# Performance work log

Measured on AMD Instinct MI355X. Metric: run time of the kernel, lower is better.

The kernel has to match this reference:

```python
import jax, jax.numpy as jnp
import numpy as np

# Dims: tokens [B,H,W,C]; 3x3 local window (NB=9 neighbors); relative-pos embed dim RP.
B, H, W, C = 4, 96, 96, 128
K, NB, RP = 3, 9, 8
HID = 128              # edge_hidden_dim = max(hidden_dim//2=128, feature_dim=128)
EDGE_IN = 3 * C + RP   # [center, neighbor, center-neighbor, rel_pos] -> 392
CLIP = 3.0
GATE_EPS = 1e-6
LN_EPS = 1e-5


def _ln(x, w, b):
    m = jnp.mean(x, axis=-1, keepdims=True)
    v = jnp.mean((x - m) ** 2, axis=-1, keepdims=True)
    return (x - m) * jax.lax.rsqrt(v + LN_EPS) * w + b


def _mlp(x, w1, b1, w2, b2):
    # Linear -> GELU (exact/erf, torch default) -> Linear; dropout is identity in eval mode.
    return jax.nn.gelu(x @ w1 + b1, approximate=False) @ w2 + b2


def _eml(drive, resistance, gamma_raw, lam, bias, warmup_eta):
    # EMLUnit energy gate (source not provided; Ohm's-law style drive/resistance,
    # positive resistance via softplus, clipped, warmup-scaled, learned bias).
    gamma = jax.nn.softplus(gamma_raw)
    conduct = drive / (jax.nn.softplus(resistance) + gamma + GATE_EPS)
    return warmup_eta * jnp.clip(lam * conduct, -CLIP, CLIP) + bias


def setup_inputs() -> dict:
    key = jax.random.key(0)
    ks = jax.random.split(key, 8)

    def w(k, shape, std=0.01):
        return jax.random.normal(k, shape, jnp.float32) * std

    return {
        "tokens": jax.random.normal(ks[0], (B, H, W, C), jnp.float32),
        "ln1_w": jnp.ones((C,), jnp.float32), "ln1_b": jnp.zeros((C,), jnp.float32),
        "ln2_w": jnp.ones((C,), jnp.float32), "ln2_b": jnp.zeros((C,), jnp.float32),
        "rel_pos": w(ks[1], (NB, RP), 0.02),
        "d_w1": w(ks[2], (EDGE_IN, HID)), "d_b1": jnp.zeros((HID,), jnp.float32),
        "d_w2": w(ks[3], (HID, 1)), "d_b2": jnp.zeros((1,), jnp.float32),
        "r_w1": w(ks[4], (EDGE_IN, HID)), "r_b1": jnp.zeros((HID,), jnp.float32),
        "r_w2": w(ks[5], (HID, 1)), "r_b2": jnp.zeros((1,), jnp.float32),
        "v_w": w(ks[6], (C, C)), "v_b": jnp.zeros((C,), jnp.float32),
        "o_w": w(ks[7], (C, C)), "o_b": jnp.zeros((C,), jnp.float32),
        "eml_gamma": jnp.full((1,), 0.1, jnp.float32),
        "eml_lam": jnp.ones((1,), jnp.float32),
        "eml_bias": jnp.full((1,), -0.3, jnp.float32),
    }


def reference(tokens, ln1_w, ln1_b, ln2_w, ln2_b, rel_pos,
              d_w1, d_b1, d_w2, d_b2, r_w1, r_b1, r_w2, r_b2,
              v_w, v_b, o_w, o_b, eml_gamma, eml_lam, eml_bias):
    b, h, w_, c = tokens.shape
    hw = h * w_
    norm = _ln(tokens, ln1_w, ln1_b)
    # nn.Unfold(kernel=3, padding=1): zero-pad then gather 3x3 windows (row-major ky,kx order).
    pad = jnp.pad(norm, ((0, 0), (1, 1), (1, 1), (0, 0)))
    neigh = jnp.stack([pad[:, dy:dy + h, dx:dx + w_, :]
                       for dy in range(K) for dx in range(K)], axis=3)  # [B,H,W,9,C]
    neigh = neigh.reshape(b, hw, NB, c)
    center = jnp.broadcast_to(norm.reshape(b, hw, 1, c), (b, hw, NB, c))
    relp = jnp.broadcast_to(rel_pos[None, None], (b, hw, NB, RP))
    edge = jnp.concatenate([center, neigh, center - neigh, relp], axis=-1)  # [B,HW,9,392]
    drive = _mlp(edge, d_w1, d_b1, d_w2, d_b2)[..., 0]        # [B,HW,9]
    resistance = _mlp(edge, r_w1, r_b1, r_w2, r_b2)[..., 0]   # [B,HW,9]
    energy = _eml(drive, resistance, eml_gamma, eml_lam, eml_bias, 1.0)
    gate = jax.nn.sigmoid(energy)[..., None]                  # [B,HW,9,1]
    values = neigh @ v_w + v_b                                # [B,HW,9,C]
    gate_mass = jnp.clip(jnp.sum(gate, axis=2), GATE_EPS, None)  # [B,HW,1]
    message = jnp.sum(gate * values, axis=2) / gate_mass      # [B,HW,C]
    update = (message @ o_w + o_b).reshape(b, h, w_, c)
    return _ln(tokens + update, ln2_w, ln2_b)
```

## Files before the change

kernel.cpp:

```cpp
#include <hip/hip_runtime.h>
#include <stdint.h>

#define NPIX 36864

using bf16x8 = __attribute__((ext_vector_type(8))) short;
using f32x4  = __attribute__((ext_vector_type(4))) float;

__device__ __forceinline__ float bf2f(uint16_t u){
  return __uint_as_float(((uint32_t)u) << 16);
}
__device__ __forceinline__ float bl(uint32_t u){ return __uint_as_float(u << 16); }
__device__ __forceinline__ float bh(uint32_t u){ return __uint_as_float(u & 0xFFFF0000u); }
__device__ __forceinline__ uint16_t f2bf(float f){
  uint32_t u = __float_as_uint(f);
  u += 0x7fffu + ((u >> 16) & 1u);
  return (uint16_t)(u >> 16);
}
__device__ __forceinline__ float ldw(const void* p, int i, bool f32){
  return f32 ? ((const float*)p)[i] : bf2f(((const uint16_t*)p)[i]);
}
__device__ __forceinline__ bool probe_f32(const void* ones_vec){
  return ((const uint32_t*)ones_vec)[0] == 0x3F800000u;
}
__device__ __forceinline__ float geluf(float x){
  float u = x * x;
  float t = x * fmaf(u, 0.0713548162f, 1.5957691216f);
  t = fminf(fmaxf(t, -30.f), 30.f);
  float e = __expf(t);
  return x * e * __builtin_amdgcn_rcpf(e + 1.0f);
}
__device__ __forceinline__ float softplusf(float x){
  return fmaxf(x, 0.f) + __logf(1.f + __expf(-fabsf(x)));
}
__device__ __forceinline__ void acc2(float& acc, uint32_t c, uint32_t n,
                                     float r0, float r1, float w0, float w1){
  acc = fmaf(geluf(bl(c) + bl(n) + r0), w0, acc);
  acc = fmaf(geluf(bh(c) + bh(n) + r1), w1, acc);
}

__global__ void prep_kernel(const void* __restrict__ dw1, const void* __restrict__ rw1,
                            const void* __restrict__ vw,  const void* __restrict__ relp,
                            const void* __restrict__ db1, const void* __restrict__ rb1,
                            const void* __restrict__ ow,  const void* __restrict__ probe,
                            const void* __restrict__ dw2, const void* __restrict__ rw2,
                            const void* __restrict__ vb,  const void* __restrict__ db2,
                            const void* __restrict__ rb2, const void* __restrict__ eg,
                            const void* __restrict__ el,  const void* __restrict__ eb,
                            uint16_t* __restrict__ wcatT, float* __restrict__ Rd,
                            float* __restrict__ Rr, uint16_t* __restrict__ owT,
                            float* __restrict__ w2df, float* __restrict__ w2rf,
                            float* __restrict__ vbf, float* __restrict__ sc){
  const bool F = probe_f32(probe);
  const int j = blockIdx.x;
  const int c = threadIdx.x;
  if (j < 640){
    float val;
    if (j < 128)      val = ldw(dw1, c*128 + j, F)             + ldw(dw1, (256+c)*128 + j, F);
    else if (j < 256) val = ldw(dw1, (128+c)*128 + (j-128), F) - ldw(dw1, (256+c)*128 + (j-128), F);
    else if (j < 384) val = ldw(rw1, c*128 + (j-256), F)       + ldw(rw1, (256+c)*128 + (j-256), F);
    else if (j < 512) val = ldw(rw1, (128+c)*128 + (j-384), F) - ldw(rw1, (256+c)*128 + (j-384), F);
    else              val = ldw(vw, c*128 + (j-512), F);
    wcatT[j*128 + c] = f2bf(val);
  } else if (j < 649){
    const int k = j - 640;
    float sd = ldw(db1, c, F);
    float sr = ldw(rb1, c, F);
    #pragma unroll
    for (int r = 0; r < 8; ++r){
      float rp = ldw(relp, k*8 + r, F);
      sd += rp * ldw(dw1, (384+r)*128 + c, F);
      sr += rp * ldw(rw1, (384+r)*128 + c, F);
    }
    Rd[k*128 + c] = sd;
    Rr[k*128 + c] = sr;
  } else if (j < 777){
    const int n = j - 649;
    owT[n*128 + c] = f2bf(ldw(ow, c*128 + n, F));
  } else {
    w2df[c] = ldw(dw2, c, F);
    w2rf[c] = ldw(rw2, c, F);
    vbf[c]  = ldw(vb, c, F);
    if (c == 0){
      sc[0] = ldw(db2, 0, F);
      sc[1] = ldw(rb2, 0, F);
      sc[2] = softplusf(ldw(eg, 0, F));
      sc[3] = ldw(el, 0, F);
      sc[4] = ldw(eb, 0, F);
    }
  }
}

__global__ __launch_bounds__(256) void ln1_kernel(const void* __restrict__ tokens,
                                                  const void* __restrict__ w,
                                                  const void* __restrict__ b,
                                                  uint16_t* __restrict__ norm){
  const bool F = probe_f32(w);
  const int wv = threadIdx.x >> 6, lane = threadIdx.x & 63;
  const int p = blockIdx.x * 4 + wv;
  float f0, f1;
  if (F){
    const float2 t = ((const float2*)tokens)[(size_t)p*64 + lane];
    f0 = t.x; f1 = t.y;
  } else {
    const uint32_t pk = ((const uint32_t*)tokens)[(size_t)p*64 + lane];
    f0 = bl(pk); f1 = bh(pk);
  }
  float s = f0 + f1;
  #pragma unroll
  for (int m = 1; m < 64; m <<= 1) s += __shfl_xor(s, m, 64);
  const float mean = s * (1.f/128.f);
  const float d0 = f0 - mean, d1 = f1 - mean;
  float q = d0*d0 + d1*d1;
  #pragma unroll
  for (int m = 1; m < 64; m <<= 1) q += __shfl_xor(q, m, 64);
  const float rs = rsqrtf(q * (1.f/128.f) + 1e-5f);
  const float n0 = d0*rs*ldw(w, 2*lane, F)   + ldw(b, 2*lane, F);
  const float n1 = d1*rs*ldw(w, 2*lane+1, F) + ldw(b, 2*lane+1, F);
  ((uint32_t*)(norm + (size_t)p*128))[lane] = (uint32_t)f2bf(n0) | ((uint32_t)f2bf(n1) << 16);
}

__global__ __launch_bounds__(256) void gemm1_kernel(const uint16_t* __restrict__ A,
                                                    const uint16_t* __restrict__ BT,
                                                    uint16_t* __restrict__ PT,
                                                    uint16_t* __restrict__ V){
  __shared__ __align__(16) uint16_t As[128*128];
  __shared__ __align__(16) uint16_t Bs[128*128];
  const int row0 = blockIdx.x * 128;
  const int s    = blockIdx.y;
  const int col0 = s * 128;
  const int t = threadIdx.x;
  #pragma unroll
  for (int i = 0; i < 8; ++i){
    int cid = t + i*256;
    int r = cid >> 4, c8 = cid & 15;
    int scz = c8 ^ (r & 15);
    *(uint4*)&As[r*128 + scz*8] = *(const uint4*)&A[(size_t)(row0+r)*128 + c8*8];
    *(uint4*)&Bs[r*128 + scz*8] = *(const uint4*)&BT[(size_t)(col0+r)*128 + c8*8];
  }
  __syncthreads();
  const int wv = t >> 6, lane = t & 63;
  const int wr = (wv >> 1) * 64, wc = (wv & 1) * 64;
  const int lr = lane & 15, quad = lane >> 4;
  f32x4 acc[4][4] = {};
  #pragma unroll
  for (int kk = 0; kk < 4; ++kk){
    const int chunk = kk*4 + quad;
    bf16x8 a[4], b[4];
    #pragma unroll
    for (int mi = 0; mi < 4; ++mi){
      int r = wr + mi*16 + lr;
      a[mi] = *(const bf16x8*)&As[r*128 + (chunk ^ (r & 15))*8];
    }
    #pragma unroll
    for (int ni = 0; ni < 4; ++ni){
      int r = wc + ni*16 + lr;
      b[ni] = *(const bf16x8*)&Bs[r*128 + (chunk ^ (r & 15))*8];
    }
    #pragma unroll
    for (int mi = 0; mi < 4; ++mi)
      #pragma unroll
      for (int ni = 0; ni < 4; ++ni)
        acc[mi][ni] = __builtin_amdgcn_mfma_f32_16x16x32_bf16(a[mi], b[ni], acc[mi][ni], 0, 0, 0);
  }
  #pragma unroll
  for (int mi = 0; mi < 4; ++mi){
    #pragma unroll
    for (int ni = 0; ni < 4; ++ni){
      const int ch   = wc + ni*16 + lr;
      const int rowb = row0 + wr + mi*16 + quad*4;
      #pragma unroll
      for (int r = 0; r < 4; ++r){
        const uint16_t vbf16 = f2bf(acc[mi][ni][r]);
        if (s < 4)
          PT[((size_t)(s*16 + (ch >> 3))*NPIX + (rowb + r))*8 + (ch & 7)] = vbf16;
        else
          V[(size_t)(rowb + r)*128 + ch] = vbf16;
      }
    }
  }
}

__global__ __launch_bounds__(192) void edge_kernel(const uint16_t* __restrict__ PTraw,
    const float* __restrict__ Rd, const float* __restrict__ Rr,
    const float* __restrict__ w2df, const float* __restrict__ w2rf,
    const float* __restrict__ sc, float* __restrict__ gates){
  const int wv = __builtin_amdgcn_readfirstlane(threadIdx.x >> 6);
  const int lane = threadIdx.x & 63;
  const int k = blockIdx.y * 3 + wv;
  const int p = blockIdx.x * 64 + lane;
  const int dy = k/3 - 1, dx = k%3 - 1;
  const int x = p % 96, y = (p / 96) % 96;
  const bool inb = ((unsigned)(x + dx) < 96u) && ((unsigned)(y + dy) < 96u);
  const uint32_t m = inb ? 0xFFFFFFFFu : 0u;
  const int q = inb ? (p + dy*96 + dx) : p;
  const uint4* PT4 = (const uint4*)PTraw;
  const float4* rd4 = (const float4*)(Rd + k*128);
  const float4* rr4 = (const float4*)(Rr + k*128);
  const float4* wd4 = (const float4*)w2df;
  const float4* wr4 = (const float4*)w2rf;
  float accd = 0.f, accr = 0.f;
  #pragma unroll 4
  for (int i = 0; i < 16; ++i){
    uint4 cd = PT4[(size_t)( 0 + i)*NPIX + p];
    uint4 nd = PT4[(size_t)(16 + i)*NPIX + q];
    uint4 cr = PT4[(size_t)(32 + i)*NPIX + p];
    uint4 nr = PT4[(size_t)(48 + i)*NPIX + q];
    nd.x &= m; nd.y &= m; nd.z &= m; nd.w &= m;
    nr.x &= m; nr.y &= m; nr.z &= m; nr.w &= m;
    const float4 rdA = rd4[2*i], rdB = rd4[2*i+1];
    const float4 rrA = rr4[2*i], rrB = rr4[2*i+1];
    const float4 wdA = wd4[2*i], wdB = wd4[2*i+1];
    const float4 wrA = wr4[2*i], wrB = wr4[2*i+1];
    acc2(accd, cd.x, nd.x, rdA.x, rdA.y, wdA.x, wdA.y);
    acc2(accd, cd.y, nd.y, rdA.z, rdA.w, wdA.z, wdA.w);
    acc2(accd, cd.z, nd.z, rdB.x, rdB.y, wdB.x, wdB.y);
    acc2(accd, cd.w, nd.w, rdB.z, rdB.w, wdB.z, wdB.w);
    acc2(accr, cr.x, nr.x, rrA.x, rrA.y, wrA.x, wrA.y);
    acc2(accr, cr.y, nr.y, rrA.z, rrA.w, wrA.z, wrA.w);
    acc2(accr, cr.z, nr.z, rrB.x, rrB.y, wrB.x, wrB.y);
    acc2(accr, cr.w, nr.w, rrB.z, rrB.w, wrB.z, wrB.w);
  }
  const float drive  = accd + sc[0];
  const float resist = accr + sc[1];
  const float cond = __fdividef(drive, softplusf(resist) + sc[2] + 1e-6f);
  const float en = fminf(fmaxf(sc[3] * cond, -3.0f), 3.0f) + sc[4];
  const float g = __fdividef(1.0f, 1.0f + __expf(-en));
  gates[(size_t)k*NPIX + p] = g;
}

__global__ __launch_bounds__(256) void msg_kernel(const uint16_t* __restrict__ V,
    const float* __restrict__ gates, const float* __restrict__ vbf,
    uint16_t* __restrict__ msg){
  const int wv = __builtin_amdgcn_readfirstlane(threadIdx.x >> 6);
  const int lane = threadIdx.x & 63;
  const int p = blockIdx.x * 4 + wv;
  const int x = p % 96, y = (p / 96) % 96;
  float g[9], gsum = 0.f;
  #pragma unroll
  for (int k = 0; k < 9; ++k){ g[k] = gates[(size_t)k*NPIX + p]; gsum += g[k]; }
  float a0 = 0.f, a1 = 0.f;
  #pragma unroll
  for (int k = 0; k < 9; ++k){
    const int dy = k/3 - 1, dx = k%3 - 1;
    if (((unsigned)(y + dy) < 96u) && ((unsigned)(x + dx) < 96u)){
      const uint32_t u = ((const uint32_t*)(V + (size_t)(p + dy*96 + dx)*128))[lane];
      a0 = fmaf(g[k], bl(u), a0);
      a1 = fmaf(g[k], bh(u), a1);
    }
  }
  const float2 vb2 = ((const float2*)vbf)[lane];
  const float inv = __fdividef(1.0f, fmaxf(gsum, 1e-6f));
  a0 = (a0 + gsum * vb2.x) * inv;
  a1 = (a1 + gsum * vb2.y) * inv;
  ((uint32_t*)(msg + (size_t)p*128))[lane] = (uint32_t)f2bf(a0) | ((uint32_t)f2bf(a1) << 16);
}

__global__ __launch_bounds__(256) void out_kernel(const uint16_t* __restrict__ Amsg,
    const uint16_t* __restrict__ owT, const void* __restrict__ tokens,
    const void* __restrict__ ob,  const void* __restrict__ ln2w,
    const void* __restrict__ ln2b, void* __restrict__ out){
  const bool F = probe_f32(ln2w);
  __shared__ __align__(16) char smem[65536];
  uint16_t* As = (uint16_t*)smem;
  uint16_t* Bs = (uint16_t*)(smem + 32768);
  float*    U  = (float*)smem;
  const int row0 = blockIdx.x * 128;
  const int t = threadIdx.x;
  #pragma unroll
  for (int i = 0; i < 8; ++i){
    int cid = t + i*256;
    int r = cid >> 4, c8 = cid & 15;
    int scz = c8 ^ (r & 15);
    *(uint4*)&As[r*128 + scz*8] = *(const uint4*)&Amsg[(size_t)(row0+r)*128 + c8*8];
    *(uint4*)&Bs[r*128 + scz*8] = *(const uint4*)&owT[(size_t)r*128 + c8*8];
  }
  __syncthreads();
  const int wv = t >> 6, lane = t & 63;
  const int wr = (wv >> 1) * 64, wc = (wv & 1) * 64;
  const int lr = lane & 15, quad = lane >> 4;
  f32x4 acc[4][4] = {};
  #pragma unroll
  for (int kk = 0; kk < 4; ++kk){
    const int chunk = kk*4 + quad;
    bf16x8 a[4], b[4];
    #pragma unroll
    for (int mi = 0; mi < 4; ++mi){
      int r = wr + mi*16 + lr;
      a[mi] = *(const bf16x8*)&As[r*128 + (chunk ^ (r & 15))*8];
    }
    #pragma unroll
    for (int ni = 0; ni < 4; ++ni){
      int r = wc + ni*16 + lr;
      b[ni] = *(const bf16x8*)&Bs[r*128 + (chunk ^ (r & 15))*8];
    }
    #pragma unroll
    for (int mi = 0; mi < 4; ++mi)
      #pragma unroll
      for (int ni = 0; ni < 4; ++ni)
        acc[mi][ni] = __builtin_amdgcn_mfma_f32_16x16x32_bf16(a[mi], b[ni], acc[mi][ni], 0, 0, 0);
  }
  __syncthreads();
  #pragma unroll
  for (int mi = 0; mi < 4; ++mi)
    #pragma unroll
    for (int ni = 0; ni < 4; ++ni)
      #pragma unroll
      for (int r = 0; r < 4; ++r)
        U[(wr + mi*16 + quad*4 + r)*128 + (wc + ni*16 + lr)] = acc[mi][ni][r];
  __syncthreads();
  const float lw0 = ldw(ln2w, 2*lane, F), lw1 = ldw(ln2w, 2*lane+1, F);
  const float lb0 = ldw(ln2b, 2*lane, F), lb1 = ldw(ln2b, 2*lane+1, F);
  const float ob0 = ldw(ob, 2*lane, F),   ob1 = ldw(ob, 2*lane+1, F);
  for (int rr = 0; rr < 32; ++rr){
    const int row = wv*32 + rr;
    const int p = row0 + row;
    const float2 uv = ((const float2*)U)[row*64 + lane];
    float t0, t1;
    if (F){
      const float2 tk = ((const float2*)tokens)[(size_t)p*64 + lane];
      t0 = tk.x; t1 = tk.y;
    } else {
      const uint32_t tk = ((const uint32_t*)tokens)[(size_t)p*64 + lane];
      t0 = bl(tk); t1 = bh(tk);
    }
    const float a0 = uv.x + ob0 + t0;
    const float a1 = uv.y + ob1 + t1;
    float s = a0 + a1;
    #pragma unroll
    for (int m = 1; m < 64; m <<= 1) s += __shfl_xor(s, m, 64);
    const float mean = s * (1.f/128.f);
    const float d0 = a0 - mean, d1 = a1 - mean;
    float q = d0*d0 + d1*d1;
    #pragma unroll
    for (int m = 1; m < 64; m <<= 1) q += __shfl_xor(q, m, 64);
    const float rs = rsqrtf(q * (1.f/128.f) + 1e-5f);
    const float o0 = d0*rs*lw0 + lb0;
    const float o1 = d1*rs*lw1 + lb1;
    if (F){
      ((float2*)out)[(size_t)p*64 + lane] = make_float2(o0, o1);
    } else {
      ((uint32_t*)out)[(size_t)p*64 + lane] = (uint32_t)f2bf(o0) | ((uint32_t)f2bf(o1) << 16);
    }
  }
}

extern "C" void kernel_launch(void* const* d_in, const int* in_sizes, int n_in,
                              void* d_out, int out_size, void* d_ws, size_t ws_size,
                              hipStream_t stream) {
  const void* tokens = d_in[0];
  const void* ln1w   = d_in[1];
  const void* ln1b   = d_in[2];
  const void* ln2w   = d_in[3];
  const void* ln2b   = d_in[4];
  const void* relp   = d_in[5];
  const void* dw1    = d_in[6];
  const void* db1    = d_in[7];
  const void* dw2    = d_in[8];
  const void* db2    = d_in[9];
  const void* rw1    = d_in[10];
  const void* rb1    = d_in[11];
  const void* rw2    = d_in[12];
  const void* rb2    = d_in[13];
  const void* vw     = d_in[14];
  const void* vb     = d_in[15];
  const void* ow     = d_in[16];
  const void* ob     = d_in[17];
  const void* eg     = d_in[18];
  const void* el     = d_in[19];
  const void* eb     = d_in[20];

  char* ws = (char*)d_ws;
  uint16_t* normb = (uint16_t*)(ws + 0);
  uint16_t* PT    = (uint16_t*)(ws + 9437184);
  uint16_t* V     = (uint16_t*)(ws + 47185920);
  float*    gates = (float*)   (ws + 56623104);
  uint16_t* wcatT = (uint16_t*)(ws + 57950208);
  float*    Rd    = (float*)   (ws + 58114048);
  float*    Rr    = (float*)   (ws + 58118656);
  uint16_t* owT   = (uint16_t*)(ws + 58123264);
  float*    w2df  = (float*)   (ws + 58156032);
  float*    w2rf  = (float*)   (ws + 58156544);
  float*    vbf   = (float*)   (ws + 58157056);
  float*    sc    = (float*)   (ws + 58157568);
  uint16_t* msg   = normb;

  prep_kernel<<<778, 128, 0, stream>>>(dw1, rw1, vw, relp, db1, rb1, ow, ln1w,
                                       dw2, rw2, vb, db2, rb2, eg, el, eb,
                                       wcatT, Rd, Rr, owT, w2df, w2rf, vbf, sc);
  ln1_kernel<<<NPIX/4, 256, 0, stream>>>(tokens, ln1w, ln1b, normb);
  gemm1_kernel<<<dim3(NPIX/128, 5), 256, 0, stream>>>(normb, wcatT, PT, V);
  edge_kernel<<<dim3(NPIX/64, 3), 192, 0, stream>>>(PT, Rd, Rr, w2df, w2rf, sc, gates);
  msg_kernel<<<NPIX/4, 256, 0, stream>>>(V, gates, vbf, msg);
  out_kernel<<<NPIX/128, 256, 0, stream>>>(msg, owT, tokens, ob, ln2w, ln2b, d_out);
}
```

Baseline: 226.8 us.

## Stage GEMM1 epilogue through LDS for coalesced stores; pipeline edge kernel loads

The GEMM1 epilogue now writes bf16 results into a padded shared-memory tile that reuses the operand buffers. The tile is then written back with 16-byte coalesced stores, replacing the scattered 2-byte global stores into the PT and V layouts. The edge kernel is remapped to a 1D grid of 256-thread blocks where each wave takes one (neighbor, strip) pair. It also prefetches the next PT chunk one iteration ahead, splits each accumulator in two for more ILP, and uses a hardware reciprocal for the sigmoid. This adds two block barriers and more registers for the prefetch.

```diff
diff --git a/kernel.cpp b/kernel.cpp
--- a/kernel.cpp
+++ b/kernel.cpp
@@ -119,12 +119,15 @@
   ((uint32_t*)(norm + (size_t)p*128))[lane] = (uint32_t)f2bf(n0) | ((uint32_t)f2bf(n1) << 16);
 }
 
+#define CSTRIDE 136
 __global__ __launch_bounds__(256) void gemm1_kernel(const uint16_t* __restrict__ A,
                                                     const uint16_t* __restrict__ BT,
                                                     uint16_t* __restrict__ PT,
                                                     uint16_t* __restrict__ V){
-  __shared__ __align__(16) uint16_t As[128*128];
-  __shared__ __align__(16) uint16_t Bs[128*128];
+  __shared__ __align__(16) char smem[65536];
+  uint16_t* As = (uint16_t*)smem;
+  uint16_t* Bs = (uint16_t*)(smem + 32768);
+  uint16_t* Cs = (uint16_t*)smem;
   const int row0 = blockIdx.x * 128;
   const int s    = blockIdx.y;
   const int col0 = s * 128;
@@ -162,32 +165,47 @@
       for (int ni = 0; ni < 4; ++ni)
         acc[mi][ni] = __builtin_amdgcn_mfma_f32_16x16x32_bf16(a[mi], b[ni], acc[mi][ni], 0, 0, 0);
   }
+  __syncthreads();
   #pragma unroll
   for (int mi = 0; mi < 4; ++mi){
     #pragma unroll
     for (int ni = 0; ni < 4; ++ni){
       const int ch   = wc + ni*16 + lr;
-      const int rowb = row0 + wr + mi*16 + quad*4;
+      const int rowb = wr + mi*16 + quad*4;
       #pragma unroll
-      for (int r = 0; r < 4; ++r){
-        const uint16_t vbf16 = f2bf(acc[mi][ni][r]);
-        if (s < 4)
-          PT[((size_t)(s*16 + (ch >> 3))*NPIX + (rowb + r))*8 + (ch & 7)] = vbf16;
-        else
-          V[(size_t)(rowb + r)*128 + ch] = vbf16;
-      }
-    }
-  }
-}
-
-__global__ __launch_bounds__(192) void edge_kernel(const uint16_t* __restrict__ PTraw,
+      for (int r = 0; r < 4; ++r)
+        Cs[(rowb + r)*CSTRIDE + ch] = f2bf(acc[mi][ni][r]);
+    }
+  }
+  __syncthreads();
+  if (s < 4){
+    #pragma unroll
+    for (int i = 0; i < 8; ++i){
+      const int idx = t + i*256;
+      const int p = idx & 127, c = idx >> 7;
+      const uint4 v = *(const uint4*)&Cs[p*CSTRIDE + c*8];
+      ((uint4*)PT)[(size_t)(s*16 + c)*NPIX + (row0 + p)] = v;
+    }
+  } else {
+    #pragma unroll
+    for (int i = 0; i < 8; ++i){
+      const int idx = t + i*256;
+      const int c8 = idx & 15, p = idx >> 4;
+      const uint4 v = *(const uint4*)&Cs[p*CSTRIDE + c8*8];
+      ((uint4*)V)[(size_t)(row0 + p)*16 + c8] = v;
+    }
+  }
+}
+
+__global__ __launch_bounds__(256) void edge_kernel(const uint16_t* __restrict__ PTraw,
     const float* __restrict__ Rd, const float* __restrict__ Rr,
     const float* __restrict__ w2df, const float* __restrict__ w2rf,
     const float* __restrict__ sc, float* __restrict__ gates){
-  const int wv = __builtin_amdgcn_readfirstlane(threadIdx.x >> 6);
-  const int lane = threadIdx.x & 63;
-  const int k = blockIdx.y * 3 + wv;
-  const int p = blockIdx.x * 64 + lane;
+  const int wv = threadIdx.x >> 6, lane = threadIdx.x & 63;
+  const int w = blockIdx.x * 4 + wv;
+  const int k = __builtin_amdgcn_readfirstlane(w % 9);
+  const int strip = __builtin_amdgcn_readfirstlane(w / 9);
+  const int p = strip * 64 + lane;
   const int dy = k/3 - 1, dx = k%3 - 1;
   const int x = p % 96, y = (p / 96) % 96;
   const bool inb = ((unsigned)(x + dx) < 96u) && ((unsigned)(y + dy) < 96u);
@@ -198,33 +216,42 @@
   const float4* rr4 = (const float4*)(Rr + k*128);
   const float4* wd4 = (const float4*)w2df;
   const float4* wr4 = (const float4*)w2rf;
-  float accd = 0.f, accr = 0.f;
-  #pragma unroll 4
+  float ad0 = 0.f, ad1 = 0.f, ar0 = 0.f, ar1 = 0.f;
+  uint4 cd = PT4[(size_t)( 0)*NPIX + p];
+  uint4 nd = PT4[(size_t)(16)*NPIX + q];
+  uint4 cr = PT4[(size_t)(32)*NPIX + p];
+  uint4 nr = PT4[(size_t)(48)*NPIX + q];
+  #pragma unroll
   for (int i = 0; i < 16; ++i){
-    uint4 cd = PT4[(size_t)( 0 + i)*NPIX + p];
-    uint4 nd = PT4[(size_t)(16 + i)*NPIX + q];
-    uint4 cr = PT4[(size_t)(32 + i)*NPIX + p];
-    uint4 nr = PT4[(size_t)(48 + i)*NPIX + q];
+    uint4 cdn, ndn, crn, nrn;
+    if (i < 15){
+      cdn = PT4[(size_t)( 0 + i+1)*NPIX + p];
+      ndn = PT4[(size_t)(16 + i+1)*NPIX + q];
+      crn = PT4[(size_t)(32 + i+1)*NPIX + p];
+      nrn = PT4[(size_t)(48 + i+1)*NPIX + q];
+    }
     nd.x &= m; nd.y &= m; nd.z &= m; nd.w &= m;
     nr.x &= m; nr.y &= m; nr.z &= m; nr.w &= m;
     const float4 rdA = rd4[2*i], rdB = rd4[2*i+1];
     const float4 rrA = rr4[2*i], rrB = rr4[2*i+1];
     const float4 wdA = wd4[2*i], wdB = wd4[2*i+1];
     const float4 wrA = wr4[2*i], wrB = wr4[2*i+1];
-    acc2(accd, cd.x, nd.x, rdA.x, rdA.y, wdA.x, wdA.y);
-    acc2(accd, cd.y, nd.y, rdA.z, rdA.w, wdA.z, wdA.w);
-    acc2(accd, cd.z, nd.z, rdB.x, rdB.y, wdB.x, wdB.y);
-    acc2(accd, cd.w, nd.w, rdB.z, rdB.w, wdB.z, wdB.w);
-    acc2(accr, cr.x, nr.x, rrA.x, rrA.y, wrA.x, wrA.y);
-    acc2(accr, cr.y, nr.y, rrA.z, rrA.w, wrA.z, wrA.w);
-    acc2(accr, cr.z, nr.z, rrB.x, rrB.y, wrB.x, wrB.y);
-    acc2(accr, cr.w, nr.w, rrB.z, rrB.w, wrB.z, wrB.w);
-  }
-  const float drive  = accd + sc[0];
-  const float resist = accr + sc[1];
+    acc2(ad0, cd.x, nd.x, rdA.x, rdA.y, wdA.x, wdA.y);
+    acc2(ad1, cd.y, nd.y, rdA.z, rdA.w, wdA.z, wdA.w);
+    acc2(ad0, cd.z, nd.z, rdB.x, rdB.y, wdB.x, wdB.y);
+    acc2(ad1, cd.w, nd.w, rdB.z, rdB.w, wdB.z, wdB.w);
+    acc2(ar0, cr.x, nr.x, rrA.x, rrA.y, wrA.x, wrA.y);
+    acc2(ar1, cr.y, nr.y, rrA.z, rrA.w, wrA.z, wrA.w);
+    acc2(ar0, cr.z, nr.z, rrB.x, rrB.y, wrB.x, wrB.y);
+    acc2(ar1, cr.w, nr.w, rrB.z, rrB.w, wrB.z, wrB.w);
+    cd = cdn; nd = ndn; cr = crn; nr = nrn;
+  }
+  const float drive  = (ad0 + ad1) + sc[0];
+  const float resist = (ar0 + ar1) + sc[1];
   const float cond = __fdividef(drive, softplusf(resist) + sc[2] + 1e-6f);
   const float en = fminf(fmaxf(sc[3] * cond, -3.0f), 3.0f) + sc[4];
-  const float g = __fdividef(1.0f, 1.0f + __expf(-en));
+  const float e = __expf(-en);
+  const float g = __builtin_amdgcn_rcpf(1.0f + e);
   gates[(size_t)k*NPIX + p] = g;
 }
 
@@ -389,7 +416,7 @@
                                        wcatT, Rd, Rr, owT, w2df, w2rf, vbf, sc);
   ln1_kernel<<<NPIX/4, 256, 0, stream>>>(tokens, ln1w, ln1b, normb);
   gemm1_kernel<<<dim3(NPIX/128, 5), 256, 0, stream>>>(normb, wcatT, PT, V);
-  edge_kernel<<<dim3(NPIX/64, 3), 192, 0, stream>>>(PT, Rd, Rr, w2df, w2rf, sc, gates);
+  edge_kernel<<<NPIX*9/256, 256, 0, stream>>>(PT, Rd, Rr, w2df, w2rf, sc, gates);
   msg_kernel<<<NPIX/4, 256, 0, stream>>>(V, gates, vbf, msg);
   out_kernel<<<NPIX/128, 256, 0, stream>>>(msg, owT, tokens, ob, ln2w, ln2b, d_out);
 }
```

Result: slower. 231.6 us (+2.1%).
